# Performance work log

Hardware: AMD Instinct MI355X
Metric: run time of the kernel (lower is better)

## Reference

```python
import jax, jax.numpy as jnp
import numpy as np

WS = 8  # window size (hardcoded in original forward)

def _window_partition(x, ws=WS):
    b, c, h, w = x.shape
    ph = (-h) % ws
    pw = (-w) % ws
    x = jnp.pad(x, ((0, 0), (0, 0), (0, ph), (0, pw)), mode='reflect')
    H, W = h + ph, w + pw
    # matches torch .view(b,c,ws,H//ws,ws,W//ws).permute(0,1,2,4,3,5)
    x = x.reshape(b, c, ws, H // ws, ws, W // ws)
    x = x.transpose(0, 1, 2, 4, 3, 5).reshape(b, c * ws * ws, H // ws, W // ws)
    return x, h, w, c, H // ws

def _l2norm_dim1(x):
    # F.normalize(x, p=2) defaults to dim=1 (token axis for [b, L, d]), eps=1e-12
    n = jnp.sqrt(jnp.sum(x * x, axis=1, keepdims=True))
    return x / jnp.maximum(n, 1e-12)

def _forward(q, k, v):
    b = q.shape[0]
    qp, qh, qw, qc, patch = _window_partition(q)
    kp, _, _, _, _ = _window_partition(k)
    vp, _, _, _, _ = _window_partition(v)
    d = qp.shape[1]  # c * ws * ws
    qt = qp.transpose(0, 2, 3, 1).reshape(b, -1, d)  # [b, L, d]
    kt = kp.transpose(0, 2, 3, 1).reshape(b, -1, d)
    vt = vp.transpose(0, 2, 3, 1).reshape(b, -1, d)
    _q = _l2norm_dim1(qt)
    _k = _l2norm_dim1(kt)
    _v = _l2norm_dim1(vt)
    sim = jnp.einsum('bld,bmd->blm', _q, _k) * (d ** -0.5)  # [b, L, L]
    out = jnp.einsum('blm,bmd->bld', jax.nn.softmax(sim, axis=-1), _v)
    # window_reverse
    L = out.shape[1]
    ws = WS
    x = out.reshape(b, patch, L // patch, qc, ws, ws)
    x = x.transpose(0, 3, 4, 1, 5, 2)  # (b, c, ws, patch, ws, L//patch)
    H = ws * patch
    x = x.reshape(b, qc, H, -1)
    return x[:, :, :qh, :qw]

def setup_inputs() -> dict:
    key = jax.random.key(0)
    kq, kk, kv = jax.random.split(key, 3)
    shape = (8, 32, 252, 252)
    return {
        'q': jax.random.normal(kq, shape, dtype=jnp.float32),
        'k': jax.random.normal(kk, shape, dtype=jnp.float32),
        'v': jax.random.normal(kv, shape, dtype=jnp.float32),
    }

def reference(q, k, v):
    return _forward(q, k, v)
```

## Files before the change

kernel.cpp:

```cpp
#include <hip/hip_runtime.h>
#include <cstdint>
#include <cstddef>


typedef __bf16 bf16x8 __attribute__((ext_vector_type(8)));
typedef float  f32x4  __attribute__((ext_vector_type(4)));

__device__ __forceinline__ unsigned short f2bf(float f) {
  unsigned int u = __builtin_bit_cast(unsigned int, f);
  u += 0x7FFFu + ((u >> 16) & 1u);
  return (unsigned short)(u >> 16);
}
__device__ __forceinline__ float bf2f(unsigned short h) {
  return __builtin_bit_cast(float, (unsigned int)h << 16);
}

__global__ void norm_kernel(const float* __restrict__ q,
                            const float* __restrict__ k,
                            const float* __restrict__ v,
                            float* __restrict__ scales) {
  int bx = blockIdx.x;
  int t   = bx >> 11;
  int rem = bx & 2047;
  int b   = rem >> 8;
  int c   = (rem >> 3) & 31;
  int i0  = rem & 7;
  const float* x = (t == 0) ? q : (t == 1) ? k : v;
  const float* base = x + ((size_t)b * 32 + c) * 63504;

  int tid = threadIdx.x;
  int w = (tid < 252) ? tid : 502 - tid;
  float s = 0.f;
  #pragma unroll 4
  for (int i1 = 0; i1 < 32; i1++) {
    int h = i0 * 32 + i1;
    int hs = (h < 252) ? h : 502 - h;
    float val = base[(size_t)hs * 252 + w];
    s += val * val;
  }
  __shared__ float red[256];
  red[tid] = s;
  __syncthreads();
  if (tid < 8) {
    float acc = 0.f;
    #pragma unroll
    for (int i = 0; i < 32; i++) acc += red[tid * 32 + i];
    float n = sqrtf(acc);
    float sc = 1.0f / fmaxf(n, 1e-12f);
    scales[((size_t)(t * 8 + b)) * 2048 + i0 * 256 + tid * 32 + c] = sc;
  }
}

__global__ void pack_kernel(const float* __restrict__ q,
                            const float* __restrict__ k,
                            const float* __restrict__ v,
                            const float* __restrict__ scales,
                            unsigned short* __restrict__ Qh,
                            unsigned short* __restrict__ Kh,
                            unsigned short* __restrict__ Vt) {
  int bx = blockIdx.x;
  int t   = bx >> 11;
  int rem = bx & 2047;
  int b   = rem >> 8;
  int i0  = (rem >> 5) & 7;
  int i1  = rem & 31;
  const float* x = (t == 0) ? q : (t == 1) ? k : v;

  __shared__ unsigned short tile[32 * 256];
  __shared__ float scl[256];

  int tid = threadIdx.x;
  scl[tid] = scales[((size_t)(t * 8 + b)) * 2048 + i0 * 256 + tid];
  __syncthreads();

  int h  = i0 * 32 + i1;
  int hs = (h < 252) ? h : 502 - h;
  int w  = tid;
  int wsrc = (w < 252) ? w : 502 - w;
  int j0 = w >> 5;
  const float* xb = x + (size_t)b * 32 * 63504;
  #pragma unroll 4
  for (int c = 0; c < 32; c++) {
    float val = xb[(size_t)c * 63504 + (size_t)hs * 252 + wsrc] * scl[j0 * 32 + c];
    tile[c * 256 + w] = f2bf(val);
  }
  __syncthreads();

  if (t < 2) {
    unsigned short* X = ((t == 0) ? Qh : Kh) + (size_t)b * 1024 * 2048;
    #pragma unroll
    for (int r = 0; r < 4; r++) {
      int g  = r * 2048 + tid * 8;
      int j1 = g >> 8;
      int p0 = g & 255;
      int j0w = p0 >> 5;
      int c0  = p0 & 31;
      unsigned int ov[4];
      #pragma unroll
      for (int m = 0; m < 4; m++) {
        unsigned int lo = tile[(c0 + 2 * m)     * 256 + j0w * 32 + j1];
        unsigned int hi = tile[(c0 + 2 * m + 1) * 256 + j0w * 32 + j1];
        ov[m] = lo | (hi << 16);
      }
      int l = i1 * 32 + j1;
      uint4 o4; o4.x = ov[0]; o4.y = ov[1]; o4.z = ov[2]; o4.w = ov[3];
      *(uint4*)&X[(size_t)l * 2048 + i0 * 256 + p0] = o4;
    }
  } else {
    unsigned short* V = Vt + (size_t)b * 2048 * 1024;
    int rrow = tid;
    int c   = rrow & 31;
    int j0r = rrow >> 5;
    unsigned short* dst = &V[(size_t)(i0 * 256 + rrow) * 1024 + i1 * 32];
    const unsigned short* src = &tile[c * 256 + j0r * 32];
    #pragma unroll
    for (int m = 0; m < 4; m++) {
      *(uint4*)&dst[m * 8] = *(const uint4*)&src[m * 8];
    }
  }
}

template <int MODE>
__global__ __launch_bounds__(256, 2)
void gemm_nt(const unsigned short* __restrict__ A,
             const unsigned short* __restrict__ B,
             int K, int Asb, int Bsb, void* __restrict__ Cout, float scale) {
  __shared__ unsigned short lA[128 * 72];
  __shared__ unsigned short lB[128 * 72];

  const int tid  = threadIdx.x;
  const int lane = tid & 63;
  const int wave = tid >> 6;
  const int ln15 = lane & 15;
  const int q4   = lane >> 4;
  const int wm   = wave >> 1;
  const int wn   = wave & 1;
  const int m0   = blockIdx.y * 128;
  const int n0   = blockIdx.x * 128;
  const unsigned short* Ab = A + (size_t)blockIdx.z * Asb;
  const unsigned short* Bb = B + (size_t)blockIdx.z * Bsb;

  f32x4 acc[4][4] = {};

  for (int k0 = 0; k0 < K; k0 += 64) {
    #pragma unroll
    for (int r = 0; r < 4; r++) {
      int id  = r * 256 + tid;
      int row = id >> 3;
      int kc  = id & 7;
      uint4 va = *(const uint4*)&Ab[(size_t)(m0 + row) * K + k0 + kc * 8];
      uint4 vb = *(const uint4*)&Bb[(size_t)(n0 + row) * K + k0 + kc * 8];
      *(uint4*)&lA[row * 72 + kc * 8] = va;
      *(uint4*)&lB[row * 72 + kc * 8] = vb;
    }
    __syncthreads();
    #pragma unroll
    for (int kk = 0; kk < 64; kk += 32) {
      bf16x8 af[4], bfr[4];
      #pragma unroll
      for (int mt = 0; mt < 4; mt++)
        af[mt] = *(const bf16x8*)&lA[(wm * 64 + mt * 16 + ln15) * 72 + kk + q4 * 8];
      #pragma unroll
      for (int nt = 0; nt < 4; nt++)
        bfr[nt] = *(const bf16x8*)&lB[(wn * 64 + nt * 16 + ln15) * 72 + kk + q4 * 8];
      #pragma unroll
      for (int mt = 0; mt < 4; mt++)
        #pragma unroll
        for (int nt = 0; nt < 4; nt++)
          acc[mt][nt] = __builtin_amdgcn_mfma_f32_16x16x32_bf16(
              af[mt], bfr[nt], acc[mt][nt], 0, 0, 0);
    }
    __syncthreads();
  }

  if (MODE == 0) {
    unsigned short* Sb = (unsigned short*)Cout + (size_t)blockIdx.z * 1024 * 1024;
    #pragma unroll
    for (int mt = 0; mt < 4; mt++) {
      #pragma unroll
      for (int nt = 0; nt < 4; nt++) {
        int col = n0 + wn * 64 + nt * 16 + ln15;
        #pragma unroll
        for (int rg = 0; rg < 4; rg++) {
          int rowi = m0 + wm * 64 + mt * 16 + q4 * 4 + rg;
          Sb[(size_t)rowi * 1024 + col] = f2bf(acc[mt][nt][rg] * scale);
        }
      }
    }
  } else {
    float* Ob = (float*)Cout;
    int bb = blockIdx.z;
    #pragma unroll
    for (int mt = 0; mt < 4; mt++) {
      #pragma unroll
      for (int nt = 0; nt < 4; nt++) {
        int l  = n0 + wn * 64 + nt * 16 + ln15;
        int i1 = l >> 5, j1 = l & 31;
        #pragma unroll
        for (int rg = 0; rg < 4; rg++) {
          int dp = m0 + wm * 64 + mt * 16 + q4 * 4 + rg;
          int c  = dp & 31;
          int j0 = (dp >> 5) & 7;
          int i0 = dp >> 8;
          int h = i0 * 32 + i1;
          int w = j0 * 32 + j1;
          if (h < 252 && w < 252)
            Ob[(((size_t)bb * 32 + c) * 252 + h) * 252 + w] = acc[mt][nt][rg];
        }
      }
    }
  }
}

__global__ void softmax_kernel(unsigned short* __restrict__ S) {
  unsigned short* row = S + (size_t)blockIdx.x * 1024;
  int tid  = threadIdx.x;
  int lane = tid & 63;
  int wid  = tid >> 6;

  uint2 u = *(const uint2*)&row[tid * 4];
  float x0 = bf2f((unsigned short)(u.x & 0xFFFF));
  float x1 = bf2f((unsigned short)(u.x >> 16));
  float x2 = bf2f((unsigned short)(u.y & 0xFFFF));
  float x3 = bf2f((unsigned short)(u.y >> 16));

  __shared__ float red[8];
  float mx = fmaxf(fmaxf(x0, x1), fmaxf(x2, x3));
  #pragma unroll
  for (int off = 32; off > 0; off >>= 1) mx = fmaxf(mx, __shfl_down(mx, off));
  if (lane == 0) red[wid] = mx;
  __syncthreads();
  if (tid == 0)
    red[4] = fmaxf(fmaxf(red[0], red[1]), fmaxf(red[2], red[3]));
  __syncthreads();
  float bm = red[4];

  float e0 = __expf(x0 - bm), e1 = __expf(x1 - bm);
  float e2 = __expf(x2 - bm), e3 = __expf(x3 - bm);
  float s = e0 + e1 + e2 + e3;
  #pragma unroll
  for (int off = 32; off > 0; off >>= 1) s += __shfl_down(s, off);
  if (lane == 0) red[wid] = s;
  __syncthreads();
  if (tid == 0) red[5] = 1.0f / (red[0] + red[1] + red[2] + red[3]);
  __syncthreads();
  float inv = red[5];

  unsigned int o0 = (unsigned int)f2bf(e0 * inv) | ((unsigned int)f2bf(e1 * inv) << 16);
  unsigned int o1 = (unsigned int)f2bf(e2 * inv) | ((unsigned int)f2bf(e3 * inv) << 16);
  uint2 o; o.x = o0; o.y = o1;
  *(uint2*)&row[tid * 4] = o;
}

extern "C" void kernel_launch(void* const* d_in, const int* in_sizes, int n_in,
                              void* d_out, int out_size, void* d_ws, size_t ws_size,
                              hipStream_t stream) {
  const float* q = (const float*)d_in[0];
  const float* k = (const float*)d_in[1];
  const float* v = (const float*)d_in[2];
  float* out = (float*)d_out;

  char* ws = (char*)d_ws;
  float* scales = (float*)ws;
  unsigned short* Qh = (unsigned short*)(ws + 196608);
  unsigned short* Kh = Qh + (size_t)8 * 1024 * 2048;
  unsigned short* Vt = Kh + (size_t)8 * 1024 * 2048;
  unsigned short* S  = Vt + (size_t)8 * 2048 * 1024;

  const float SIM_SCALE = 0.02209708691207961f;

  norm_kernel<<<6144, 256, 0, stream>>>(q, k, v, scales);
  pack_kernel<<<6144, 256, 0, stream>>>(q, k, v, scales, Qh, Kh, Vt);
  gemm_nt<0><<<dim3(8, 8, 8), 256, 0, stream>>>(
      Qh, Kh, 2048, 1024 * 2048, 1024 * 2048, (void*)S, SIM_SCALE);
  softmax_kernel<<<8192, 256, 0, stream>>>(S);
  gemm_nt<1><<<dim3(8, 16, 8), 256, 0, stream>>>(
      Vt, S, 1024, 2048 * 1024, 1024 * 1024, (void*)out, 1.0f);
}
```

Baseline: 404.1 us.

## Vectorize norm/pack loads and use direct global-to-LDS loads with XOR swizzle in GEMM

The norm and pack kernels now read the inputs with float4 vector loads and handle the reflect padding through per-chunk weights and a special tail chunk, instead of issuing scalar per-element reflected loads. The GEMM stages tiles with global_load_lds directly into an unpadded LDS layout that uses an XOR swizzle to avoid bank conflicts. The smaller LDS footprint allows launch bounds to be raised to 4 blocks per CU. The goal is to cut global load instruction count and register staging. The risks are subtle reflect-index errors and higher register pressure under the tighter occupancy target.

Result: faster. 392.0 us (-3.0%).

```diff
diff --git a/kernel.cpp b/kernel.cpp
--- a/kernel.cpp
+++ b/kernel.cpp
@@ -6,13 +6,19 @@
 typedef __bf16 bf16x8 __attribute__((ext_vector_type(8)));
 typedef float  f32x4  __attribute__((ext_vector_type(4)));
 
-__device__ __forceinline__ unsigned short f2bf(float f) {
+__device__ __forceinline__ unsigned int f2bf(float f) {
   unsigned int u = __builtin_bit_cast(unsigned int, f);
   u += 0x7FFFu + ((u >> 16) & 1u);
-  return (unsigned short)(u >> 16);
+  return u >> 16;
 }
 __device__ __forceinline__ float bf2f(unsigned short h) {
   return __builtin_bit_cast(float, (unsigned int)h << 16);
+}
+
+__device__ __forceinline__ void load_lds16(const void* g, void* l) {
+  __builtin_amdgcn_global_load_lds(
+      (const __attribute__((address_space(1))) void*)g,
+      (__attribute__((address_space(3))) void*)l, 16, 0, 0);
 }
 
 __global__ void norm_kernel(const float* __restrict__ q,
@@ -28,15 +34,29 @@
   const float* x = (t == 0) ? q : (t == 1) ? k : v;
   const float* base = x + ((size_t)b * 32 + c) * 63504;
 
-  int tid = threadIdx.x;
-  int w = (tid < 252) ? tid : 502 - tid;
+  int tid   = threadIdx.x;
+  int chunk = tid & 63;
+  int i1b   = tid >> 6;
+
+  float cw0 = 1.f, cw1 = 1.f, cw2 = 1.f, cw3 = 1.f;
+  bool skipc = false;
+  if (chunk == 61) cw3 = 2.f;
+  else if (chunk == 62) { cw0 = cw1 = cw2 = 2.f; }
+  else if (chunk == 63) skipc = true;
+
   float s = 0.f;
-  #pragma unroll 4
-  for (int i1 = 0; i1 < 32; i1++) {
-    int h = i0 * 32 + i1;
-    int hs = (h < 252) ? h : 502 - h;
-    float val = base[(size_t)hs * 252 + w];
-    s += val * val;
+  if (!skipc) {
+    #pragma unroll
+    for (int r = 0; r < 8; r++) {
+      int i1 = r * 4 + i1b;
+      int h  = i0 * 32 + i1;
+      if (h < 252) {
+        float rw = (i0 == 7 && h >= 247 && h <= 250) ? 2.f : 1.f;
+        float4 vv = *(const float4*)&base[(size_t)h * 252 + chunk * 4];
+        s += rw * (cw0 * vv.x * vv.x + cw1 * vv.y * vv.y +
+                   cw2 * vv.z * vv.z + cw3 * vv.w * vv.w);
+      }
+    }
   }
   __shared__ float red[256];
   red[tid] = s;
@@ -44,9 +64,10 @@
   if (tid < 8) {
     float acc = 0.f;
     #pragma unroll
-    for (int i = 0; i < 32; i++) acc += red[tid * 32 + i];
-    float n = sqrtf(acc);
-    float sc = 1.0f / fmaxf(n, 1e-12f);
+    for (int w = 0; w < 4; w++)
+      #pragma unroll
+      for (int e = 0; e < 8; e++) acc += red[w * 64 + tid * 8 + e];
+    float sc = 1.0f / fmaxf(sqrtf(acc), 1e-12f);
     scales[((size_t)(t * 8 + b)) * 2048 + i0 * 256 + tid * 32 + c] = sc;
   }
 }
@@ -75,14 +96,29 @@
 
   int h  = i0 * 32 + i1;
   int hs = (h < 252) ? h : 502 - h;
-  int w  = tid;
-  int wsrc = (w < 252) ? w : 502 - w;
-  int j0 = w >> 5;
-  const float* xb = x + (size_t)b * 32 * 63504;
-  #pragma unroll 4
-  for (int c = 0; c < 32; c++) {
-    float val = xb[(size_t)c * 63504 + (size_t)hs * 252 + wsrc] * scl[j0 * 32 + c];
-    tile[c * 256 + w] = f2bf(val);
+  const float* xb = x + (size_t)b * 32 * 63504 + (size_t)hs * 252;
+
+  #pragma unroll
+  for (int r = 0; r < 8; r++) {
+    int idx   = r * 256 + tid;
+    int c     = idx >> 6;
+    int chunk = idx & 63;
+    const float* src = xb + (size_t)c * 63504;
+    if (chunk < 63) {
+      float sc = scl[(chunk >> 3) * 32 + c];
+      float4 vv = *(const float4*)&src[chunk * 4];
+      uint2 o;
+      o.x = f2bf(vv.x * sc) | (f2bf(vv.y * sc) << 16);
+      o.y = f2bf(vv.z * sc) | (f2bf(vv.w * sc) << 16);
+      *(uint2*)&tile[c * 256 + chunk * 4] = o;
+    } else {
+      float sc = scl[7 * 32 + c];
+      float a0 = src[250], a1 = src[249], a2 = src[248], a3 = src[247];
+      uint2 o;
+      o.x = f2bf(a0 * sc) | (f2bf(a1 * sc) << 16);
+      o.y = f2bf(a2 * sc) | (f2bf(a3 * sc) << 16);
+      *(uint2*)&tile[c * 256 + 252] = o;
+    }
   }
   __syncthreads();
 
@@ -121,12 +157,12 @@
 }
 
 template <int MODE>
-__global__ __launch_bounds__(256, 2)
+__global__ __launch_bounds__(256, 4)
 void gemm_nt(const unsigned short* __restrict__ A,
              const unsigned short* __restrict__ B,
              int K, int Asb, int Bsb, void* __restrict__ Cout, float scale) {
-  __shared__ unsigned short lA[128 * 72];
-  __shared__ unsigned short lB[128 * 72];
+  __shared__ unsigned short lA[128 * 64];
+  __shared__ unsigned short lB[128 * 64];
 
   const int tid  = threadIdx.x;
   const int lane = tid & 63;
@@ -140,29 +176,36 @@
   const unsigned short* Ab = A + (size_t)blockIdx.z * Asb;
   const unsigned short* Bb = B + (size_t)blockIdx.z * Bsb;
 
+  const int srow = lane >> 3;
+  const int kcp  = lane & 7;
+  const int kcl  = kcp ^ srow;
+
   f32x4 acc[4][4] = {};
 
   for (int k0 = 0; k0 < K; k0 += 64) {
     #pragma unroll
     for (int r = 0; r < 4; r++) {
-      int id  = r * 256 + tid;
-      int row = id >> 3;
-      int kc  = id & 7;
-      uint4 va = *(const uint4*)&Ab[(size_t)(m0 + row) * K + k0 + kc * 8];
-      uint4 vb = *(const uint4*)&Bb[(size_t)(n0 + row) * K + k0 + kc * 8];
-      *(uint4*)&lA[row * 72 + kc * 8] = va;
-      *(uint4*)&lB[row * 72 + kc * 8] = vb;
+      int rowg = wave * 32 + r * 8;
+      int row  = rowg + srow;
+      load_lds16(&Ab[(size_t)(m0 + row) * K + k0 + kcl * 8], &lA[rowg * 64]);
+      load_lds16(&Bb[(size_t)(n0 + row) * K + k0 + kcl * 8], &lB[rowg * 64]);
     }
     __syncthreads();
     #pragma unroll
-    for (int kk = 0; kk < 64; kk += 32) {
+    for (int kk = 0; kk < 2; kk++) {
       bf16x8 af[4], bfr[4];
       #pragma unroll
-      for (int mt = 0; mt < 4; mt++)
-        af[mt] = *(const bf16x8*)&lA[(wm * 64 + mt * 16 + ln15) * 72 + kk + q4 * 8];
-      #pragma unroll
-      for (int nt = 0; nt < 4; nt++)
-        bfr[nt] = *(const bf16x8*)&lB[(wn * 64 + nt * 16 + ln15) * 72 + kk + q4 * 8];
+      for (int mt = 0; mt < 4; mt++) {
+        int row = wm * 64 + mt * 16 + ln15;
+        int pc  = (kk * 4 + q4) ^ (row & 7);
+        af[mt] = *(const bf16x8*)&lA[row * 64 + pc * 8];
+      }
+      #pragma unroll
+      for (int nt = 0; nt < 4; nt++) {
+        int row = wn * 64 + nt * 16 + ln15;
+        int pc  = (kk * 4 + q4) ^ (row & 7);
+        bfr[nt] = *(const bf16x8*)&lB[row * 64 + pc * 8];
+      }
       #pragma unroll
       for (int mt = 0; mt < 4; mt++)
         #pragma unroll
@@ -183,7 +226,7 @@
         #pragma unroll
         for (int rg = 0; rg < 4; rg++) {
           int rowi = m0 + wm * 64 + mt * 16 + q4 * 4 + rg;
-          Sb[(size_t)rowi * 1024 + col] = f2bf(acc[mt][nt][rg] * scale);
+          Sb[(size_t)rowi * 1024 + col] = (unsigned short)f2bf(acc[mt][nt][rg] * scale);
         }
       }
     }
@@ -246,8 +289,8 @@
   __syncthreads();
   float inv = red[5];
 
-  unsigned int o0 = (unsigned int)f2bf(e0 * inv) | ((unsigned int)f2bf(e1 * inv) << 16);
-  unsigned int o1 = (unsigned int)f2bf(e2 * inv) | ((unsigned int)f2bf(e3 * inv) << 16);
+  unsigned int o0 = f2bf(e0 * inv) | (f2bf(e1 * inv) << 16);
+  unsigned int o1 = f2bf(e2 * inv) | (f2bf(e3 * inv) << 16);
   uint2 o; o.x = o0; o.y = o1;
   *(uint2*)&row[tid * 4] = o;
 }
```
